# Kernel optimization log

Hardware: AMD Instinct MI355X
Metric: run time of the kernel (lower is better)

## Reference

```python
import jax, jax.numpy as jnp
import numpy as np

B, T, CNN, HW = 512, 256, 512, 7
V, H = 37, 8  # vocab_size, hidden_size


def setup_inputs() -> dict:
    key = jax.random.key(0)
    ks = jax.random.split(key, 10)
    s = 0.1
    return {
        "features": jax.random.normal(ks[0], (B, CNN, HW, HW), jnp.float32),
        "captions": jax.random.normal(ks[1], (B, T, V), jnp.float32),
        "W_in": jax.random.normal(ks[2], (V, CNN), jnp.float32) * s,
        "b_in": jax.random.normal(ks[3], (V,), jnp.float32) * s,
        "W_ih": jax.random.normal(ks[4], (4 * H, V), jnp.float32) * s,
        "W_hh": jax.random.normal(ks[5], (4 * H, H), jnp.float32) * s,
        "b_ih": jax.random.normal(ks[6], (4 * H,), jnp.float32) * s,
        "b_hh": jax.random.normal(ks[7], (4 * H,), jnp.float32) * s,
        "W_out": jax.random.normal(ks[8], (V, H), jnp.float32) * s,
        "b_out": jax.random.normal(ks[9], (V,), jnp.float32) * s,
    }


def reference(features, captions, W_in, b_in, W_ih, W_hh, b_ih, b_hh, W_out, b_out):
    # AdaptiveAvgPool2d(1) + flatten + fc_in -> [B, V]
    feat = features.mean(axis=(2, 3)) @ W_in.T + b_in
    # input at t=0 is feat, at t>0 is captions[:, t-1]; build [T, B, V] sequence
    xs = jnp.concatenate([feat[None], jnp.swapaxes(captions, 0, 1)[:-1]], axis=0)

    def step(carry, x):
        h, c = carry
        gates = x @ W_ih.T + b_ih + h @ W_hh.T + b_hh  # [B, 4H]
        i, f, g, o = jnp.split(gates, 4, axis=1)  # PyTorch LSTMCell gate order
        i = jax.nn.sigmoid(i)
        f = jax.nn.sigmoid(f)
        g = jnp.tanh(g)
        o = jax.nn.sigmoid(o)
        c = f * c + i * g
        h = o * jnp.tanh(c)
        out = jax.nn.softmax(h @ W_out.T + b_out, axis=1)  # [B, V]
        return (h, c), out

    h0 = jnp.zeros((feat.shape[0], W_hh.shape[1]), feat.dtype)
    c0 = jnp.zeros_like(h0)
    _, outs = jax.lax.scan(step, (h0, c0), xs)  # outs: [T, B, V]
    return jnp.swapaxes(outs, 0, 1)  # [B, T, V]
```

## Files before the change

### kernel.cpp

```cpp
#include <hip/hip_runtime.h>
#include <math.h>

#define BB   512
#define TT   256
#define CNNC 512
#define VV   37
#define HH   8
#define G4   32
#define CH   32
#define CW   (CH * 128)

#define L2E 1.4426950408889634f

typedef float f4_t __attribute__((ext_vector_type(4)));

__device__ __forceinline__ void async_copy16(const float* g, float* l) {
    __builtin_amdgcn_global_load_lds(
        (__attribute__((address_space(1))) void*)g,
        (__attribute__((address_space(3))) void*)l, 16, 0, 0);
}

template <int CTRL>
__device__ __forceinline__ float dpp_f(float x) {
    int r = __builtin_amdgcn_update_dpp(0, __float_as_int(x), CTRL, 0xF, 0xF, true);
    return __int_as_float(r);
}

__device__ __forceinline__ float rcp_f(float x) { return __builtin_amdgcn_rcpf(x); }
__device__ __forceinline__ float exp2_f(float x) { return __builtin_amdgcn_exp2f(x); }

__global__ __launch_bounds__(256) void k_feat(const float* __restrict__ features,
                                              const float* __restrict__ W_in,
                                              const float* __restrict__ b_in,
                                              float* __restrict__ featp) {
    __shared__ __align__(16) float raw[128 * 49];
    __shared__ float pooled[128];
    const int b = blockIdx.x, qt = blockIdx.y, tid = threadIdx.x;
    const f4_t* src =
        (const f4_t*)(features + (size_t)b * CNNC * 49 + qt * (128 * 49));
    f4_t* dst = (f4_t*)raw;
    for (int i = tid; i < 128 * 49 / 4; i += 256)
        dst[i] = __builtin_nontemporal_load(&src[i]);
    __syncthreads();
    if (tid < 128) {
        const float* p = raw + tid * 49;
        float s = 0.f;
        #pragma unroll
        for (int i = 0; i < 49; ++i) s += p[i];
        pooled[tid] = s;
    }
    __syncthreads();
    const int v = tid >> 2, pp = tid & 3;
    if (v < VV) {
        const float* w = W_in + v * CNNC + qt * 128 + pp * 32;
        const float* q = pooled + pp * 32;
        float s = 0.f;
        #pragma unroll
        for (int i = 0; i < 32; ++i) s += q[i] * w[i];
        s += __shfl_xor(s, 1);
        s += __shfl_xor(s, 2);
        if (pp == 0)
            featp[(qt * BB + b) * VV + v] =
                s * (1.f / 49.f) + (qt == 0 ? b_in[v] : 0.f);
    }
}

#define CAPS 1188
#define SOS  132
__global__ __launch_bounds__(256) void k_xproj(const float* __restrict__ captions,
                                               const float* __restrict__ W_ih,
                                               const float* __restrict__ b_ih,
                                               const float* __restrict__ b_hh,
                                               const float* __restrict__ featp,
                                               float* __restrict__ xproj) {
    __shared__ float W[G4 * VV];
    __shared__ float bias[G4];
    __shared__ float cap[4 * CAPS];
    __shared__ __align__(16) float so[32 * SOS];
    const int bg = blockIdx.x, tile = blockIdx.y;
    const int tid = threadIdx.x;
    for (int i = tid; i < G4 * VV; i += 256) W[i] = W_ih[i];
    if (tid < G4) bias[tid] = b_ih[tid] + b_hh[tid];

    const int t0 = tile * 32;
    const int start = (tile == 0) ? 0 : t0 - 1;
    for (int i = tid; i < 4 * 1184; i += 256) {
        const int s2 = i / 1184;
        const int off = i - s2 * 1184;
        cap[s2 * CAPS + off] = __builtin_nontemporal_load(
            &captions[((size_t)(bg * 4 + s2) * TT + start) * VV + off]);
    }
    __syncthreads();

    const int tl = tid >> 3;
    const int s  = (tid >> 1) & 3;
    const int r  = tid & 1;
    const int t  = t0 + tl;
    const int b  = bg * 4 + s;

    float xr[VV];
    if (tile == 0 && tl == 0) {
        #pragma unroll
        for (int v = 0; v < VV; ++v)
            xr[v] = featp[b * VV + v] + featp[(BB + b) * VV + v] +
                    featp[(2 * BB + b) * VV + v] + featp[(3 * BB + b) * VV + v];
    } else {
        const int lr = (tile == 0) ? tl - 1 : tl;
        const float* x = &cap[s * CAPS + lr * VV];
        #pragma unroll
        for (int v = 0; v < VV; ++v) xr[v] = x[v];
    }

    const int g0 = r * 16;
    float acc[16];
    #pragma unroll
    for (int g = 0; g < 16; ++g) acc[g] = bias[g0 + g];
    #pragma unroll
    for (int v = 0; v < VV; ++v) {
        const float xv = xr[v];
        #pragma unroll
        for (int g = 0; g < 16; ++g) acc[g] += xv * W[(g0 + g) * VV + v];
    }
    #pragma unroll
    for (int g = 0; g < 16; ++g) {
        const int gg = g0 + g;
        const float sc = (gg >= 16 && gg < 24) ? (-2.f * L2E) : (-L2E);
        so[tl * SOS + gg * 4 + s] = acc[g] * sc;
    }
    __syncthreads();

    float* chunk = xproj + ((size_t)bg * TT + t0) * 128;
    for (int i = tid; i < 1024; i += 256) {
        const int t2 = i >> 5, rest = i & 31;
        f4_t val = *(const f4_t*)&so[t2 * SOS + rest * 4];
        *(f4_t*)&chunk[t2 * 128 + rest * 4] = val;
    }
}

__global__ __launch_bounds__(192) void k_lstm(const float* __restrict__ W_hh,
                                              const float* __restrict__ xproj,
                                              const float* __restrict__ W_out,
                                              const float* __restrict__ b_out,
                                              float* __restrict__ out) {
    __shared__ __align__(16) float buf[3 * CW + 128];
    __shared__ __align__(16) float hst[2 * 4 * CH * HH];
    __shared__ __align__(16) float Wo[VV * HH];
    __shared__ float bo[VV];

    const int tid  = threadIdx.x;
    const int wv   = tid >> 6;
    const int lane = tid & 63;
    const int bg   = blockIdx.x;
    const float* xp = xproj + (size_t)bg * (TT * 128);

    if (wv == 0) {
        #pragma unroll
        for (int it = 0; it < 16; ++it)
            async_copy16(xp + (it * 64 + lane) * 4, &buf[it * 256]);
        #pragma unroll
        for (int it = 0; it < 16; ++it)
            async_copy16(xp + CW + (it * 64 + lane) * 4, &buf[CW + it * 256]);
    } else {
        const int l2 = tid - 64;
        for (int i = l2; i < VV * HH; i += 128) Wo[i] = W_out[i];
        if (l2 < VV) bo[l2] = b_out[l2];
    }

    const int s4 = lane >> 4;
    const int q  = lane & 15;
    const int j  = q >> 1;
    const int r  = q & 1;
    float wA[HH], wB[HH];
    int roff = 0;
    if (wv == 0) {
        const int rowA = r * 8 + j;
        const int rowB = 16 + r * 8 + j;
        const float scA = -L2E;
        const float scB = r ? -L2E : (-2.f * L2E);
        #pragma unroll
        for (int m = 0; m < HH; ++m) {
            wA[m] = scA * W_hh[rowA * HH + (j ^ m)];
            wB[m] = scB * W_hh[rowB * HH + (j ^ m)];
        }
        roff = rowA * 4 + s4;
    }
    float h = 0.f, c = 0.f;

    const int orow = (wv - 1) * 64 + lane;
    const int os   = orow >> 5;
    const int otl  = orow & 31;

    for (int it = 0; it < 9; ++it) {
        if (wv == 0) {
            if (it < 8) {
                if (it == 0)      asm volatile("s_waitcnt vmcnt(16)" ::: "memory");
                else if (it == 7) asm volatile("s_waitcnt vmcnt(32)" ::: "memory");
                else              asm volatile("s_waitcnt vmcnt(48)" ::: "memory");

                const float* base = &buf[(it % 3) * CW] + roff;
                float* hsl = &hst[((it & 1) * 4 + s4) * (CH * HH) + j];
                float pA = base[0], pB = base[64];
                #pragma unroll
                for (int tl = 0; tl < CH; ++tl) {
                    const float nA = base[(tl + 1) * 128];
                    const float nB = base[(tl + 1) * 128 + 64];

                    const float ha0 = h;
                    const float ha1 = dpp_f<0x4E>(h);
                    const float ha3 = dpp_f<0x141>(h);
                    const float ha2 = dpp_f<0x4E>(ha3);
                    const float ha7 = dpp_f<0x140>(h);
                    const float ha4 = dpp_f<0x141>(ha7);
                    const float ha5 = dpp_f<0x4E>(ha4);
                    const float ha6 = dpp_f<0x1B>(ha7);

                    float a0 = fmaf(wA[0], ha0, pA);
                    a0 = fmaf(wA[1], ha1, a0);
                    a0 = fmaf(wA[2], ha2, a0);
                    a0 = fmaf(wA[3], ha3, a0);
                    float a1 = wA[4] * ha4;
                    a1 = fmaf(wA[5], ha5, a1);
                    a1 = fmaf(wA[6], ha6, a1);
                    a1 = fmaf(wA[7], ha7, a1);
                    const float npA = a0 + a1;
                    float b0 = fmaf(wB[0], ha0, pB);
                    b0 = fmaf(wB[1], ha1, b0);
                    b0 = fmaf(wB[2], ha2, b0);
                    b0 = fmaf(wB[3], ha3, b0);
                    float b1 = wB[4] * ha4;
                    b1 = fmaf(wB[5], ha5, b1);
                    b1 = fmaf(wB[6], ha6, b1);
                    b1 = fmaf(wB[7], ha7, b1);
                    const float npB = b0 + b1;

                    const float eA = rcp_f(1.f + exp2_f(npA));
                    const float uB = rcp_f(1.f + exp2_f(npB));
                    const float gg = fmaf(-4.f * L2E, uB, 2.f * L2E);

                    const float myU = r ? eA : eA * gg;
                    const float otU = dpp_f<0xB1>(myU);
                    const float fg  = r ? myU : otU;
                    const float igg = r ? otU : myU;
                    const float ogx = dpp_f<0xB1>(uB);
                    const float og  = r ? uB : ogx;

                    c = fmaf(fg, c, igg);
                    const float th = fmaf(2.f, rcp_f(1.f + exp2_f(c)), -1.f);
                    h = og * th;
                    if (r == 0) hsl[tl * HH] = h;
                    pA = nA; pB = nB;
                }
                if (it + 2 < TT / CH) {
                    const float* src = xp + (size_t)(it + 2) * CW;
                    float* db = &buf[((it + 2) % 3) * CW];
                    #pragma unroll
                    for (int k = 0; k < 16; ++k)
                        async_copy16(src + (k * 64 + lane) * 4, &db[k * 256]);
                }
            }
        } else if (it >= 1) {
            const int pk = it - 1;
            const f4_t* hp =
                (const f4_t*)&hst[(((pk & 1) * 4 + os) * CH + otl) * HH];
            const f4_t h0 = hp[0], h1 = hp[1];
            const f4_t* W4 = (const f4_t*)Wo;
            float z[VV];
            float m = -1e30f;
            #pragma unroll
            for (int v = 0; v < VV; ++v) {
                const f4_t w0 = W4[v * 2], w1 = W4[v * 2 + 1];
                float sv = bo[v];
                sv = fmaf(h0.x, w0.x, sv); sv = fmaf(h0.y, w0.y, sv);
                sv = fmaf(h0.z, w0.z, sv); sv = fmaf(h0.w, w0.w, sv);
                sv = fmaf(h1.x, w1.x, sv); sv = fmaf(h1.y, w1.y, sv);
                sv = fmaf(h1.z, w1.z, sv); sv = fmaf(h1.w, w1.w, sv);
                z[v] = sv;
                m = fmaxf(m, sv);
            }
            float sum = 0.f;
            #pragma unroll
            for (int v = 0; v < VV; ++v) {
                z[v] = exp2_f((z[v] - m) * L2E);
                sum += z[v];
            }
            const float rs = rcp_f(sum);
            const int b = bg * 4 + os;
            const int t = pk * CH + otl;
            float* op = out + ((size_t)b * TT + t) * VV;
            #pragma unroll
            for (int v = 0; v < VV; ++v) op[v] = z[v] * rs;
        }
        asm volatile("s_waitcnt lgkmcnt(0)" ::: "memory");
        __builtin_amdgcn_s_barrier();
        __builtin_amdgcn_sched_barrier(0);
    }
}

extern "C" void kernel_launch(void* const* d_in, const int* in_sizes, int n_in,
                              void* d_out, int out_size, void* d_ws, size_t ws_size,
                              hipStream_t stream) {
    const float* features = (const float*)d_in[0];
    const float* captions = (const float*)d_in[1];
    const float* W_in     = (const float*)d_in[2];
    const float* b_in     = (const float*)d_in[3];
    const float* W_ih     = (const float*)d_in[4];
    const float* W_hh     = (const float*)d_in[5];
    const float* b_ih     = (const float*)d_in[6];
    const float* b_hh     = (const float*)d_in[7];
    const float* W_out    = (const float*)d_in[8];
    const float* b_out    = (const float*)d_in[9];
    float* out = (float*)d_out;

    float* ws    = (float*)d_ws;
    float* featp = ws;
    float* xproj = ws + 81920;

    k_feat <<<dim3(BB, 4),  256, 0, stream>>>(features, W_in, b_in, featp);
    k_xproj<<<dim3(128, 8), 256, 0, stream>>>(captions, W_ih, b_ih, b_hh, featp, xproj);
    k_lstm <<<128,          192, 0, stream>>>(W_hh, xproj, W_out, b_out, out);
}
```

Baseline: 194.3 us.

## Prefetch xproj into registers with interleaved layout, drop LDS async staging

Interleaves the two gate-projection values per row in the xproj layout so each recurrence lane reads a float2 straight from global memory into a register double-buffer, replacing the LDS async-copy triple buffer and its manual vmcnt waits. The chunk size is halved to 16 steps, h values are kept in registers and flushed to padded LDS once per chunk, and the softmax output is handled by one wave instead of two (block shrinks from 192 to 128 threads). The goal is to take LDS reads and waitcnt stalls off the serial recurrence critical path. The trade-offs are register pressure from the register buffers, twice as many barriers, and a smaller output wave that may not keep up with the recurrence.

```diff
diff --git a/kernel.cpp b/kernel.cpp
--- a/kernel.cpp
+++ b/kernel.cpp
@@ -7,18 +7,14 @@
 #define VV   37
 #define HH   8
 #define G4   32
-#define CH   32
-#define CW   (CH * 128)
+#define CH   16
+#define NCH  (TT / CH)
+#define CHW  (CH * 128)
 
 #define L2E 1.4426950408889634f
 
 typedef float f4_t __attribute__((ext_vector_type(4)));
-
-__device__ __forceinline__ void async_copy16(const float* g, float* l) {
-    __builtin_amdgcn_global_load_lds(
-        (__attribute__((address_space(1))) void*)g,
-        (__attribute__((address_space(3))) void*)l, 16, 0, 0);
-}
+typedef float f2_t __attribute__((ext_vector_type(2)));
 
 template <int CTRL>
 __device__ __forceinline__ float dpp_f(float x) {
@@ -95,7 +91,6 @@
     const int tl = tid >> 3;
     const int s  = (tid >> 1) & 3;
     const int r  = tid & 1;
-    const int t  = t0 + tl;
     const int b  = bg * 4 + s;
 
     float xr[VV];
@@ -125,7 +120,8 @@
     for (int g = 0; g < 16; ++g) {
         const int gg = g0 + g;
         const float sc = (gg >= 16 && gg < 24) ? (-2.f * L2E) : (-L2E);
-        so[tl * SOS + gg * 4 + s] = acc[g] * sc;
+        const int word = ((gg & 15) * 4 + s) * 2 + (gg >> 4);
+        so[tl * SOS + word] = acc[g] * sc;
     }
     __syncthreads();
 
@@ -137,13 +133,108 @@
     }
 }
 
-__global__ __launch_bounds__(192) void k_lstm(const float* __restrict__ W_hh,
+#define TSTR 12
+#define SSTR (CH * TSTR + 4)
+
+#define STEP(cur, tl) do {                                                  \
+    const float pA = cur[tl].x, pB = cur[tl].y;                             \
+    const float ha0 = h;                                                    \
+    const float ha1 = dpp_f<0x4E>(h);                                       \
+    const float ha3 = dpp_f<0x141>(h);                                      \
+    const float ha2 = dpp_f<0x4E>(ha3);                                     \
+    const float ha7 = dpp_f<0x140>(h);                                      \
+    const float ha4 = dpp_f<0x141>(ha7);                                    \
+    const float ha5 = dpp_f<0x4E>(ha4);                                     \
+    const float ha6 = dpp_f<0x1B>(ha7);                                     \
+    float a0 = fmaf(wA[0], ha0, pA);                                        \
+    a0 = fmaf(wA[1], ha1, a0);                                              \
+    a0 = fmaf(wA[2], ha2, a0);                                              \
+    a0 = fmaf(wA[3], ha3, a0);                                              \
+    float a1 = wA[4] * ha4;                                                 \
+    a1 = fmaf(wA[5], ha5, a1);                                              \
+    a1 = fmaf(wA[6], ha6, a1);                                              \
+    a1 = fmaf(wA[7], ha7, a1);                                              \
+    const float npA = a0 + a1;                                              \
+    float b0 = fmaf(wB[0], ha0, pB);                                        \
+    b0 = fmaf(wB[1], ha1, b0);                                              \
+    b0 = fmaf(wB[2], ha2, b0);                                              \
+    b0 = fmaf(wB[3], ha3, b0);                                              \
+    float b1 = wB[4] * ha4;                                                 \
+    b1 = fmaf(wB[5], ha5, b1);                                              \
+    b1 = fmaf(wB[6], ha6, b1);                                              \
+    b1 = fmaf(wB[7], ha7, b1);                                              \
+    const float npB = b0 + b1;                                              \
+    const float eA = rcp_f(1.f + exp2_f(npA));         \
+    const float uB = rcp_f(1.f + exp2_f(npB));     \
+    const float gg = fmaf(-4.f * L2E, uB, 2.f * L2E);    \
+    const float myU = r ? eA : eA * gg;           \
+    const float otU = dpp_f<0xB1>(myU);                                     \
+    const float fg  = r ? myU : otU;                                        \
+    const float igg = r ? otU : myU;                                        \
+    const float ogx = dpp_f<0xB1>(uB);                                      \
+    const float og  = r ? uB : ogx;                                         \
+    c = fmaf(fg, c, igg);                         \
+    const float rv = rcp_f(1.f + exp2_f(c));                                \
+    const float og2 = og + og;                                              \
+    h = fmaf(og2, rv, -og);                                 \
+    hsv[tl] = h;                                                            \
+} while (0)
+
+#define CHUNK(cur, nxt, it, pbuf) do {                                      \
+    if ((it) + 1 < NCH) {                                                   \
+        const f2_t* src = (const f2_t*)(xp + ((it) + 1) * CHW + roff2);     \
+        _Pragma("unroll")                                                   \
+        for (int tl = 0; tl < CH; ++tl) nxt[tl] = src[tl * 64];             \
+        __builtin_amdgcn_sched_barrier(0);                                  \
+    }                                                                       \
+    _Pragma("unroll")                                                       \
+    for (int tl = 0; tl < CH; ++tl) STEP(cur, tl);                          \
+    if (r == 0) {                                                           \
+        float* hb = &hst[((pbuf) * 4 + s4) * SSTR + j];                     \
+        _Pragma("unroll")                                                   \
+        for (int i = 0; i < CH; ++i) hb[i * TSTR] = hsv[i];                 \
+    }                                                                       \
+} while (0)
+
+#define EMIT(pk) do {                                                       \
+    const int os = lane >> 4, otl = lane & 15;                              \
+    const float* hp = &hst[(((pk) & 1) * 4 + os) * SSTR + otl * TSTR];      \
+    const f4_t h0 = *(const f4_t*)hp;                                       \
+    const f4_t h1 = *(const f4_t*)(hp + 4);                                 \
+    const f4_t* W4 = (const f4_t*)Wo;                                       \
+    float z[VV];                                                            \
+    float m = -1e30f;                                                       \
+    _Pragma("unroll")                                                       \
+    for (int v = 0; v < VV; ++v) {                                          \
+        const f4_t w0 = W4[v * 2], w1 = W4[v * 2 + 1];                      \
+        float sv = bo[v];                                                   \
+        sv = fmaf(h0.x, w0.x, sv); sv = fmaf(h0.y, w0.y, sv);               \
+        sv = fmaf(h0.z, w0.z, sv); sv = fmaf(h0.w, w0.w, sv);               \
+        sv = fmaf(h1.x, w1.x, sv); sv = fmaf(h1.y, w1.y, sv);               \
+        sv = fmaf(h1.z, w1.z, sv); sv = fmaf(h1.w, w1.w, sv);               \
+        z[v] = sv;                                                          \
+        m = fmaxf(m, sv);                                                   \
+    }                                                                       \
+    float sum = 0.f;                                                        \
+    _Pragma("unroll")                                                       \
+    for (int v = 0; v < VV; ++v) {                                          \
+        z[v] = exp2_f((z[v] - m) * L2E);                                    \
+        sum += z[v];                                                        \
+    }                                                                       \
+    const float rs = rcp_f(sum);                                            \
+    const int ob = bg * 4 + os;                                             \
+    const int ot = (pk) * CH + otl;                                         \
+    float* op = out + ((size_t)ob * TT + ot) * VV;                          \
+    _Pragma("unroll")                                                       \
+    for (int v = 0; v < VV; ++v) op[v] = z[v] * rs;                         \
+} while (0)
+
+__global__ __launch_bounds__(128) void k_lstm(const float* __restrict__ W_hh,
                                               const float* __restrict__ xproj,
                                               const float* __restrict__ W_out,
                                               const float* __restrict__ b_out,
                                               float* __restrict__ out) {
-    __shared__ __align__(16) float buf[3 * CW + 128];
-    __shared__ __align__(16) float hst[2 * 4 * CH * HH];
+    __shared__ __align__(16) float hst[2 * 4 * SSTR];
     __shared__ __align__(16) float Wo[VV * HH];
     __shared__ float bo[VV];
 
@@ -153,28 +244,19 @@
     const int bg   = blockIdx.x;
     const float* xp = xproj + (size_t)bg * (TT * 128);
 
-    if (wv == 0) {
-        #pragma unroll
-        for (int it = 0; it < 16; ++it)
-            async_copy16(xp + (it * 64 + lane) * 4, &buf[it * 256]);
-        #pragma unroll
-        for (int it = 0; it < 16; ++it)
-            async_copy16(xp + CW + (it * 64 + lane) * 4, &buf[CW + it * 256]);
-    } else {
-        const int l2 = tid - 64;
-        for (int i = l2; i < VV * HH; i += 128) Wo[i] = W_out[i];
-        if (l2 < VV) bo[l2] = b_out[l2];
-    }
-
     const int s4 = lane >> 4;
     const int q  = lane & 15;
     const int j  = q >> 1;
     const int r  = q & 1;
+    const int rowA  = r * 8 + j;
+    const int roff2 = (rowA * 4 + s4) * 2;
+
+    f2_t cA[CH], cB[CH];
+    float hsv[CH];
     float wA[HH], wB[HH];
-    int roff = 0;
+
     if (wv == 0) {
-        const int rowA = r * 8 + j;
-        const int rowB = 16 + r * 8 + j;
+        const int rowB = 16 + rowA;
         const float scA = -L2E;
         const float scB = r ? -L2E : (-2.f * L2E);
         #pragma unroll
@@ -182,117 +264,41 @@
             wA[m] = scA * W_hh[rowA * HH + (j ^ m)];
             wB[m] = scB * W_hh[rowB * HH + (j ^ m)];
         }
-        roff = rowA * 4 + s4;
-    }
+        const f2_t* src = (const f2_t*)(xp + roff2);
+        #pragma unroll
+        for (int tl = 0; tl < CH; ++tl) cA[tl] = src[tl * 64];
+    } else {
+        for (int i = lane; i < VV * HH; i += 64) Wo[i] = W_out[i];
+        if (lane < VV) bo[lane] = b_out[lane];
+    }
+
     float h = 0.f, c = 0.f;
 
-    const int orow = (wv - 1) * 64 + lane;
-    const int os   = orow >> 5;
-    const int otl  = orow & 31;
-
-    for (int it = 0; it < 9; ++it) {
-        if (wv == 0) {
-            if (it < 8) {
-                if (it == 0)      asm volatile("s_waitcnt vmcnt(16)" ::: "memory");
-                else if (it == 7) asm volatile("s_waitcnt vmcnt(32)" ::: "memory");
-                else              asm volatile("s_waitcnt vmcnt(48)" ::: "memory");
-
-                const float* base = &buf[(it % 3) * CW] + roff;
-                float* hsl = &hst[((it & 1) * 4 + s4) * (CH * HH) + j];
-                float pA = base[0], pB = base[64];
-                #pragma unroll
-                for (int tl = 0; tl < CH; ++tl) {
-                    const float nA = base[(tl + 1) * 128];
-                    const float nB = base[(tl + 1) * 128 + 64];
-
-                    const float ha0 = h;
-                    const float ha1 = dpp_f<0x4E>(h);
-                    const float ha3 = dpp_f<0x141>(h);
-                    const float ha2 = dpp_f<0x4E>(ha3);
-                    const float ha7 = dpp_f<0x140>(h);
-                    const float ha4 = dpp_f<0x141>(ha7);
-                    const float ha5 = dpp_f<0x4E>(ha4);
-                    const float ha6 = dpp_f<0x1B>(ha7);
-
-                    float a0 = fmaf(wA[0], ha0, pA);
-                    a0 = fmaf(wA[1], ha1, a0);
-                    a0 = fmaf(wA[2], ha2, a0);
-                    a0 = fmaf(wA[3], ha3, a0);
-                    float a1 = wA[4] * ha4;
-                    a1 = fmaf(wA[5], ha5, a1);
-                    a1 = fmaf(wA[6], ha6, a1);
-                    a1 = fmaf(wA[7], ha7, a1);
-                    const float npA = a0 + a1;
-                    float b0 = fmaf(wB[0], ha0, pB);
-                    b0 = fmaf(wB[1], ha1, b0);
-                    b0 = fmaf(wB[2], ha2, b0);
-                    b0 = fmaf(wB[3], ha3, b0);
-                    float b1 = wB[4] * ha4;
-                    b1 = fmaf(wB[5], ha5, b1);
-                    b1 = fmaf(wB[6], ha6, b1);
-                    b1 = fmaf(wB[7], ha7, b1);
-                    const float npB = b0 + b1;
-
-                    const float eA = rcp_f(1.f + exp2_f(npA));
-                    const float uB = rcp_f(1.f + exp2_f(npB));
-                    const float gg = fmaf(-4.f * L2E, uB, 2.f * L2E);
-
-                    const float myU = r ? eA : eA * gg;
-                    const float otU = dpp_f<0xB1>(myU);
-                    const float fg  = r ? myU : otU;
-                    const float igg = r ? otU : myU;
-                    const float ogx = dpp_f<0xB1>(uB);
-                    const float og  = r ? uB : ogx;
-
-                    c = fmaf(fg, c, igg);
-                    const float th = fmaf(2.f, rcp_f(1.f + exp2_f(c)), -1.f);
-                    h = og * th;
-                    if (r == 0) hsl[tl * HH] = h;
-                    pA = nA; pB = nB;
+    for (int ou = 0; ou < 9; ++ou) {
+        {
+            const int it = ou * 2;
+            if (wv == 0) {
+                if (it < NCH) CHUNK(cA, cB, it, 0);
+            } else if (it >= 1 && it <= NCH) {
+                EMIT(it - 1);
+            }
+            asm volatile("s_waitcnt lgkmcnt(0)" ::: "memory");
+            __builtin_amdgcn_s_barrier();
+            __builtin_amdgcn_sched_barrier(0);
+        }
+        {
+            const int it = ou * 2 + 1;
+            if (it <= NCH) {
+                if (wv == 0) {
+                    if (it < NCH) CHUNK(cB, cA, it, 1);
+                } else {
+                    EMIT(it - 1);
                 }
-                if (it + 2 < TT / CH) {
-                    const float* src = xp + (size_t)(it + 2) * CW;
-                    float* db = &buf[((it + 2) % 3) * CW];
-                    #pragma unroll
-                    for (int k = 0; k < 16; ++k)
-                        async_copy16(src + (k * 64 + lane) * 4, &db[k * 256]);
-                }
+                asm volatile("s_waitcnt lgkmcnt(0)" ::: "memory");
+                __builtin_amdgcn_s_barrier();
+                __builtin_amdgcn_sched_barrier(0);
             }
-        } else if (it >= 1) {
-            const int pk = it - 1;
-            const f4_t* hp =
-                (const f4_t*)&hst[(((pk & 1) * 4 + os) * CH + otl) * HH];
-            const f4_t h0 = hp[0], h1 = hp[1];
-            const f4_t* W4 = (const f4_t*)Wo;
-            float z[VV];
-            float m = -1e30f;
-            #pragma unroll
-            for (int v = 0; v < VV; ++v) {
-                const f4_t w0 = W4[v * 2], w1 = W4[v * 2 + 1];
-                float sv = bo[v];
-                sv = fmaf(h0.x, w0.x, sv); sv = fmaf(h0.y, w0.y, sv);
-                sv = fmaf(h0.z, w0.z, sv); sv = fmaf(h0.w, w0.w, sv);
-                sv = fmaf(h1.x, w1.x, sv); sv = fmaf(h1.y, w1.y, sv);
-                sv = fmaf(h1.z, w1.z, sv); sv = fmaf(h1.w, w1.w, sv);
-                z[v] = sv;
-                m = fmaxf(m, sv);
-            }
-            float sum = 0.f;
-            #pragma unroll
-            for (int v = 0; v < VV; ++v) {
-                z[v] = exp2_f((z[v] - m) * L2E);
-                sum += z[v];
-            }
-            const float rs = rcp_f(sum);
-            const int b = bg * 4 + os;
-            const int t = pk * CH + otl;
-            float* op = out + ((size_t)b * TT + t) * VV;
-            #pragma unroll
-            for (int v = 0; v < VV; ++v) op[v] = z[v] * rs;
         }
-        asm volatile("s_waitcnt lgkmcnt(0)" ::: "memory");
-        __builtin_amdgcn_s_barrier();
-        __builtin_amdgcn_sched_barrier(0);
     }
 }
 
@@ -317,5 +323,5 @@
 
     k_feat <<<dim3(BB, 4),  256, 0, stream>>>(features, W_in, b_in, featp);
     k_xproj<<<dim3(128, 8), 256, 0, stream>>>(captions, W_ih, b_ih, b_hh, featp, xproj);
-    k_lstm <<<128,          192, 0, stream>>>(W_hh, xproj, W_out, b_out, out);
-}
+    k_lstm <<<128,          128, 0, stream>>>(W_hh, xproj, W_out, b_out, out);
+}
```

Measured after the change: 192.2 us. Within noise of the previous version (-1.1%).
